# Performance work log

Measured on AMD Instinct MI355X. Metric: run time of the kernel, lower is better.

The kernel has to match this reference:

```python
import jax, jax.numpy as jnp
import numpy as np

NUM_USERS = 50000
NUM_ITEMS = 20000
NUM_NODES = NUM_USERS + NUM_ITEMS
FEAT_DIM = 768
HID = 128
NUM_LAYERS = 3
N_EDGES = 2_000_000
LN_EPS = 1e-5


def setup_inputs() -> dict:
    key = jax.random.key(0)
    ks = jax.random.split(key, 12)
    edge_index = jax.random.randint(ks[0], (2, N_EDGES), 0, NUM_NODES, dtype=jnp.int64) if jax.config.jax_enable_x64 else jax.random.randint(ks[0], (2, N_EDGES), 0, NUM_NODES, dtype=jnp.int32)
    item_features = jax.random.normal(ks[1], (NUM_ITEMS, FEAT_DIM), dtype=jnp.float32)
    embedding = jax.random.normal(ks[2], (NUM_NODES, HID), dtype=jnp.float32) * 0.1
    W1 = jax.random.normal(ks[3], (FEAT_DIM, 512), dtype=jnp.float32) * 0.02
    b1 = jnp.zeros((512,), jnp.float32)
    g1 = jnp.ones((512,), jnp.float32)
    be1 = jnp.zeros((512,), jnp.float32)
    W2 = jax.random.normal(ks[4], (512, HID), dtype=jnp.float32) * 0.02
    b2 = jnp.zeros((HID,), jnp.float32)
    g2 = jnp.ones((HID,), jnp.float32)
    be2 = jnp.zeros((HID,), jnp.float32)
    W3 = jax.random.normal(ks[5], (HID, HID), dtype=jnp.float32) * 0.02
    b3 = jnp.zeros((HID,), jnp.float32)
    meta_weight = jnp.asarray(0.01, jnp.float32)
    return {"edge_index": edge_index, "item_features": item_features, "embedding": embedding,
            "W1": W1, "b1": b1, "g1": g1, "be1": be1,
            "W2": W2, "b2": b2, "g2": g2, "be2": be2,
            "W3": W3, "b3": b3, "meta_weight": meta_weight}


def _layer_norm(x, g, b):
    mu = jnp.mean(x, axis=-1, keepdims=True)
    var = jnp.mean(jnp.square(x - mu), axis=-1, keepdims=True)
    return (x - mu) * jax.lax.rsqrt(var + LN_EPS) * g + b


def reference(edge_index, item_features, embedding, W1, b1, g1, be1, W2, b2, g2, be2, W3, b3, meta_weight):
    # item metadata MLP (eval mode: dropout is identity)
    h = jax.nn.relu(_layer_norm(item_features @ W1 + b1, g1, be1))
    h = jax.nn.relu(_layer_norm(h @ W2 + b2, g2, be2))
    h = h @ W3 + b3
    # F.normalize(p=2, dim=-1)
    item_meta = h / jnp.maximum(jnp.linalg.norm(h, axis=-1, keepdims=True), 1e-12)

    # fuse metadata into item id embeddings
    e0 = jnp.concatenate([embedding[:NUM_USERS],
                          embedding[NUM_USERS:] + meta_weight * item_meta], axis=0)

    src, dst = edge_index[0], edge_index[1]
    # symmetric GCN normalization: deg from destination counts
    deg = jax.ops.segment_sum(jnp.ones(src.shape[0], e0.dtype), dst, num_segments=NUM_NODES)
    dinv = jnp.where(deg > 0, jax.lax.rsqrt(jnp.maximum(deg, 1.0)), 0.0)
    norm = (dinv[src] * dinv[dst])[:, None]  # [E, 1]

    alpha = 1.0 / (NUM_LAYERS + 1)
    out = e0 * alpha
    x = e0
    for _ in range(NUM_LAYERS):
        x = jax.ops.segment_sum(x[src] * norm, dst, num_segments=NUM_NODES)
        out = out + x * alpha
    return out
```

## Files before the change

kernel.cpp:

```cpp
#include <hip/hip_runtime.h>
#include <hip/hip_bf16.h>

#define NUM_USERS 50000
#define NUM_ITEMS 20000
#define NUM_NODES (NUM_USERS + NUM_ITEMS)
#define FEAT_DIM 768
#define HID 128
#define H1DIM 512
#define LN_EPS 1e-5f
#define ALPHA 0.25f
#define NBKT 137

typedef __attribute__((ext_vector_type(8))) short short8;
typedef __attribute__((ext_vector_type(4))) float floatx4;

static __device__ inline unsigned short f2bf(float f) {
  unsigned int u = __float_as_uint(f);
  u += 0x7fffu + ((u >> 16) & 1u);
  return (unsigned short)(u >> 16);
}
static __device__ inline float bflo(unsigned int u) {
  return __uint_as_float(u << 16);
}
static __device__ inline float bfhi(unsigned int u) {
  return __uint_as_float(u & 0xffff0000u);
}

__global__ __launch_bounds__(256) void cast_bf16(
    const float* __restrict__ in, unsigned short* __restrict__ out) {
  size_t i = (size_t)blockIdx.x * 256 + threadIdx.x;
  float4 u = ((const float4*)in)[i * 2];
  float4 v = ((const float4*)in)[i * 2 + 1];
  union { unsigned short s[8]; uint4 q; } p;
  p.s[0] = f2bf(u.x); p.s[1] = f2bf(u.y); p.s[2] = f2bf(u.z); p.s[3] = f2bf(u.w);
  p.s[4] = f2bf(v.x); p.s[5] = f2bf(v.y); p.s[6] = f2bf(v.z); p.s[7] = f2bf(v.w);
  ((uint4*)out)[i] = p.q;
}

__global__ __launch_bounds__(256) void transpose_cast(
    const float* __restrict__ W, unsigned short* __restrict__ Wt,
    int K, int N) {
  __shared__ float tile[32][33];
  int tx = threadIdx.x, ty = threadIdx.y;
  int bx = blockIdx.x, by = blockIdx.y;
#pragma unroll
  for (int kk = 0; kk < 4; kk++)
    tile[ty + kk * 8][tx] = W[(size_t)(by * 32 + ty + kk * 8) * N + bx * 32 + tx];
  __syncthreads();
#pragma unroll
  for (int kk = 0; kk < 4; kk++)
    Wt[(size_t)(bx * 32 + ty + kk * 8) * K + by * 32 + tx] =
        f2bf(tile[tx][ty + kk * 8]);
}

__global__ __launch_bounds__(256) void gemm_mfma_bias(
    const unsigned short* __restrict__ A, const unsigned short* __restrict__ Bt,
    const float* __restrict__ bias, float* __restrict__ C,
    int M, int N, int K) {
  __shared__ __align__(16) unsigned short As[128 * 32];
  __shared__ __align__(16) unsigned short Bs[128 * 32];
  const int tid = threadIdx.x;
  const int wave = tid >> 6, lane = tid & 63;
  const int quad = lane >> 4, l16 = lane & 15;
  const int wm = wave >> 1, wn = wave & 1;
  const int bm = blockIdx.y * 128, bn = blockIdx.x * 128;

  floatx4 acc[4][4];
#pragma unroll
  for (int i = 0; i < 4; i++)
#pragma unroll
    for (int j = 0; j < 4; j++) acc[i][j] = (floatx4){0.f, 0.f, 0.f, 0.f};

  const int srow = lane >> 2;
  const int scol = (lane & 3) * 8;

  for (int k0 = 0; k0 < K; k0 += 32) {
#pragma unroll
    for (int i = 0; i < 2; i++) {
      int c = wave * 2 + i;
      int arow = bm + c * 16 + srow;
      if (arow >= M) arow = M - 1;
      const unsigned short* ga = A + (size_t)arow * K + k0 + scol;
      __builtin_amdgcn_global_load_lds(
          (const __attribute__((address_space(1))) unsigned int*)(uintptr_t)ga,
          (__attribute__((address_space(3))) unsigned int*)(uintptr_t)(As + c * 512),
          16, 0, 0);
      int brow = bn + c * 16 + srow;
      const unsigned short* gb = Bt + (size_t)brow * K + k0 + scol;
      __builtin_amdgcn_global_load_lds(
          (const __attribute__((address_space(1))) unsigned int*)(uintptr_t)gb,
          (__attribute__((address_space(3))) unsigned int*)(uintptr_t)(Bs + c * 512),
          16, 0, 0);
    }
    __syncthreads();

    short8 af[4], bf[4];
#pragma unroll
    for (int i = 0; i < 4; i++) {
      af[i] = *(const short8*)&As[(wm * 64 + i * 16 + l16) * 32 + quad * 8];
      bf[i] = *(const short8*)&Bs[(wn * 64 + i * 16 + l16) * 32 + quad * 8];
    }
#pragma unroll
    for (int i = 0; i < 4; i++)
#pragma unroll
      for (int j = 0; j < 4; j++)
        acc[i][j] = __builtin_amdgcn_mfma_f32_16x16x32_bf16(af[i], bf[j],
                                                            acc[i][j], 0, 0, 0);
    __syncthreads();
  }

#pragma unroll
  for (int i = 0; i < 4; i++) {
    int row0 = bm + wm * 64 + i * 16 + quad * 4;
#pragma unroll
    for (int j = 0; j < 4; j++) {
      int col = bn + wn * 64 + j * 16 + l16;
      float bv = bias[col];
#pragma unroll
      for (int r = 0; r < 4; r++) {
        int row = row0 + r;
        if (row < M) C[(size_t)row * N + col] = acc[i][j][r] + bv;
      }
    }
  }
}

__global__ __launch_bounds__(256) void ln_relu_w512_bf16(
    const float* __restrict__ X, const float* __restrict__ g,
    const float* __restrict__ be, unsigned short* __restrict__ O) {
  int row = blockIdx.x, t = threadIdx.x;
  const float* x = X + (size_t)row * H1DIM;
  float v0 = x[t], v1 = x[t + 256];
  float s = v0 + v1, q = v0 * v0 + v1 * v1;
#pragma unroll
  for (int off = 32; off > 0; off >>= 1) {
    s += __shfl_down(s, off);
    q += __shfl_down(q, off);
  }
  __shared__ float ss[4], qq[4];
  int lane = t & 63, wid = t >> 6;
  if (lane == 0) { ss[wid] = s; qq[wid] = q; }
  __syncthreads();
  float S = ss[0] + ss[1] + ss[2] + ss[3];
  float Q = qq[0] + qq[1] + qq[2] + qq[3];
  float mu = S * (1.f / 512.f);
  float var = Q * (1.f / 512.f) - mu * mu;
  float rs = rsqrtf(var + LN_EPS);
  float y0 = (v0 - mu) * rs * g[t] + be[t];
  float y1 = (v1 - mu) * rs * g[t + 256] + be[t + 256];
  unsigned short* o = O + (size_t)row * H1DIM;
  o[t] = f2bf(fmaxf(y0, 0.f));
  o[t + 256] = f2bf(fmaxf(y1, 0.f));
}

__global__ __launch_bounds__(256) void ln_relu_w128(
    float* __restrict__ X, const float* __restrict__ g,
    const float* __restrict__ be, int rows) {
  int gwid = (blockIdx.x * blockDim.x + threadIdx.x) >> 6;
  if (gwid >= rows) return;
  int lane = threadIdx.x & 63;
  float* x = X + (size_t)gwid * HID;
  float v0 = x[lane], v1 = x[lane + 64];
  float s = v0 + v1, q = v0 * v0 + v1 * v1;
#pragma unroll
  for (int off = 32; off > 0; off >>= 1) {
    s += __shfl_down(s, off);
    q += __shfl_down(q, off);
  }
  s = __shfl(s, 0);
  q = __shfl(q, 0);
  float mu = s * (1.f / 128.f);
  float var = q * (1.f / 128.f) - mu * mu;
  float rs = rsqrtf(var + LN_EPS);
  float y0 = (v0 - mu) * rs * g[lane] + be[lane];
  float y1 = (v1 - mu) * rs * g[lane + 64] + be[lane + 64];
  x[lane] = fmaxf(y0, 0.f);
  x[lane + 64] = fmaxf(y1, 0.f);
}

__global__ __launch_bounds__(128) void gemm3_norm4(
    const float* __restrict__ H, const float* __restrict__ W3,
    const float* __restrict__ b3, float* __restrict__ meta) {
  int r0 = blockIdx.x * 4, t = threadIdx.x;
  __shared__ float hrow[4][HID];
#pragma unroll
  for (int r = 0; r < 4; r++) hrow[r][t] = H[(size_t)(r0 + r) * HID + t];
  __syncthreads();
  float s0 = 0.f, s1 = 0.f, s2 = 0.f, s3 = 0.f;
#pragma unroll 4
  for (int k = 0; k < HID; k++) {
    float w = W3[k * HID + t];
    s0 = fmaf(hrow[0][k], w, s0);
    s1 = fmaf(hrow[1][k], w, s1);
    s2 = fmaf(hrow[2][k], w, s2);
    s3 = fmaf(hrow[3][k], w, s3);
  }
  float b = b3[t];
  s0 += b; s1 += b; s2 += b; s3 += b;
  float q0 = s0 * s0, q1 = s1 * s1, q2 = s2 * s2, q3 = s3 * s3;
#pragma unroll
  for (int off = 32; off > 0; off >>= 1) {
    q0 += __shfl_down(q0, off);
    q1 += __shfl_down(q1, off);
    q2 += __shfl_down(q2, off);
    q3 += __shfl_down(q3, off);
  }
  __shared__ float qs[4][2];
  if ((t & 63) == 0) {
    int w = t >> 6;
    qs[0][w] = q0; qs[1][w] = q1; qs[2][w] = q2; qs[3][w] = q3;
  }
  __syncthreads();
  float n0 = fmaxf(sqrtf(qs[0][0] + qs[0][1]), 1e-12f);
  float n1 = fmaxf(sqrtf(qs[1][0] + qs[1][1]), 1e-12f);
  float n2 = fmaxf(sqrtf(qs[2][0] + qs[2][1]), 1e-12f);
  float n3 = fmaxf(sqrtf(qs[3][0] + qs[3][1]), 1e-12f);
  meta[(size_t)(r0 + 0) * HID + t] = s0 / n0;
  meta[(size_t)(r0 + 1) * HID + t] = s1 / n1;
  meta[(size_t)(r0 + 2) * HID + t] = s2 / n2;
  meta[(size_t)(r0 + 3) * HID + t] = s3 / n3;
}

__global__ __launch_bounds__(256) void build_e0_cm4(
    const float* __restrict__ emb, const float* __restrict__ meta,
    const float* __restrict__ mw_p, const float* __restrict__ dinv,
    unsigned int* __restrict__ x0c, float* __restrict__ out) {
  size_t i = (size_t)blockIdx.x * 256 + threadIdx.x;
  int node = (int)(i >> 6);
  int u6 = (int)(i & 63);
  int chunk = u6 >> 4, fl = u6 & 15;
  int f0 = chunk * 32 + fl * 2;
  float2 e = *(const float2*)&emb[(size_t)node * HID + f0];
  if (node >= NUM_USERS) {
    float2 m = *(const float2*)&meta[(size_t)(node - NUM_USERS) * HID + f0];
    float w = mw_p[0];
    e.x += w * m.x;
    e.y += w * m.y;
  }
  *(float2*)&out[(size_t)node * HID + f0] = make_float2(ALPHA * e.x, ALPHA * e.y);
  float d = dinv[node];
  unsigned pk = (unsigned)f2bf(d * e.x) | ((unsigned)f2bf(d * e.y) << 16);
  x0c[((size_t)chunk * NUM_NODES + node) * 16 + fl] = pk;
}

__global__ __launch_bounds__(256) void p1_hist(const int* __restrict__ dst,
                                               int* __restrict__ ghist,
                                               int E, int NBL) {
  __shared__ int h[NBKT];
  int t = threadIdx.x;
  if (t < NBKT) h[t] = 0;
  __syncthreads();
  int base = blockIdx.x * 8192;
  for (int i = t; i < 8192; i += 256) {
    int e = base + i;
    if (e < E) atomicAdd(&h[dst[e] >> 9], 1);
  }
  __syncthreads();
  if (t < NBKT) ghist[t * NBL + blockIdx.x] = h[t];
}

__global__ __launch_bounds__(256) void scan_a(const int* __restrict__ in,
                                              int* __restrict__ outp,
                                              int* __restrict__ bsum, int n) {
  int i = blockIdx.x * 256 + threadIdx.x;
  int v = (i < n) ? in[i] : 0;
  int lane = threadIdx.x & 63, wid = threadIdx.x >> 6;
  int s = v;
#pragma unroll
  for (int off = 1; off < 64; off <<= 1) {
    int u = __shfl_up(s, off);
    if (lane >= off) s += u;
  }
  __shared__ int wsum[4];
  if (lane == 63) wsum[wid] = s;
  __syncthreads();
  int add = 0;
  for (int w = 0; w < wid; w++) add += wsum[w];
  int incl = s + add;
  if (i < n) outp[i] = incl - v;
  if (threadIdx.x == 255) bsum[blockIdx.x] = incl;
}

__global__ __launch_bounds__(512) void scan_b(int* __restrict__ bsum, int nb) {
  int t = threadIdx.x;
  int v = (t < nb) ? bsum[t] : 0;
  int lane = t & 63, wid = t >> 6;
  int s = v;
#pragma unroll
  for (int off = 1; off < 64; off <<= 1) {
    int u = __shfl_up(s, off);
    if (lane >= off) s += u;
  }
  __shared__ int ws[8];
  if (lane == 63) ws[wid] = s;
  __syncthreads();
  int add = 0;
  for (int w = 0; w < wid; w++) add += ws[w];
  if (t < nb) bsum[t] = s + add - v;
}

__global__ __launch_bounds__(256) void scan_c(int* __restrict__ outp,
                                              const int* __restrict__ bsum,
                                              int n) {
  int i = blockIdx.x * 256 + threadIdx.x;
  if (i < n) outp[i] += bsum[blockIdx.x];
}

__global__ __launch_bounds__(256) void p1_scatter(
    const int* __restrict__ src, const int* __restrict__ dst,
    const int* __restrict__ gscan, unsigned long long* __restrict__ pairs,
    int E, int NBL) {
  __shared__ int cur[NBKT];
  int t = threadIdx.x;
  if (t < NBKT) cur[t] = gscan[t * NBL + blockIdx.x];
  __syncthreads();
  int base = blockIdx.x * 8192;
  for (int i = t; i < 8192; i += 256) {
    int e = base + i;
    if (e < E) {
      int d = dst[e];
      int pos = atomicAdd(&cur[d >> 9], 1);
      pairs[pos] = ((unsigned long long)(unsigned)d << 32) | (unsigned)src[e];
    }
  }
}

__global__ __launch_bounds__(512) void p2_build(
    const unsigned long long* __restrict__ pairs,
    const int* __restrict__ gscan, int* __restrict__ rowptr,
    int* __restrict__ csr_src, int E, int NBL) {
  __shared__ int hist[512];
  __shared__ int ws8[8];
  int b = blockIdx.x, t = threadIdx.x;
  int base = gscan[b * NBL];
  int end = (b == NBKT - 1) ? E : gscan[(b + 1) * NBL];
  hist[t] = 0;
  __syncthreads();
  for (int i = base + t; i < end; i += 512) {
    unsigned d = (unsigned)(pairs[i] >> 32);
    atomicAdd(&hist[d & 511], 1);
  }
  __syncthreads();
  int v = hist[t];
  int lane = t & 63, wid = t >> 6;
  int s = v;
#pragma unroll
  for (int off = 1; off < 64; off <<= 1) {
    int u = __shfl_up(s, off);
    if (lane >= off) s += u;
  }
  if (lane == 63) ws8[wid] = s;
  __syncthreads();
  int add = 0;
  for (int w = 0; w < wid; w++) add += ws8[w];
  int excl = s + add - v;
  int node = (b << 9) + t;
  if (node < NUM_NODES) rowptr[node] = base + excl;
  if (b == NBKT - 1 && t == 0) rowptr[NUM_NODES] = E;
  __syncthreads();
  hist[t] = base + excl;
  __syncthreads();
  for (int i = base + t; i < end; i += 512) {
    unsigned long long p = pairs[i];
    unsigned d = (unsigned)(p >> 32);
    int pos = atomicAdd(&hist[d & 511], 1);
    csr_src[pos] = (int)(unsigned)p;
  }
}

__global__ __launch_bounds__(256) void calc_dinv2(const int* __restrict__ rowptr,
                                                  float* __restrict__ dinv,
                                                  int n) {
  int i = blockIdx.x * 256 + threadIdx.x;
  if (i < n) {
    int d = rowptr[i + 1] - rowptr[i];
    dinv[i] = d > 0 ? rsqrtf((float)d) : 0.f;
  }
}

#define ACC1(v)                 \
  {                             \
    a0 += bflo((v).x);          \
    a1 += bfhi((v).x);          \
    a2 += bflo((v).y);          \
    a3 += bfhi((v).y);          \
  }

__global__ __launch_bounds__(256) void spmm_chunk4(
    const int* __restrict__ rowptr, const int* __restrict__ csrc,
    const float* __restrict__ dinv, const uint2* __restrict__ xc,
    uint2* __restrict__ yc, float* __restrict__ out, int write_y) {
  int chunk = blockIdx.x & 3;
  int rowblk = blockIdx.x >> 2;
  int tid = threadIdx.x;
  int wave = tid >> 6, lane = tid & 63;
  int slot = lane >> 3, fl = lane & 7;
  int row = rowblk * 32 + wave * 8 + slot;
  bool act = row < NUM_NODES;
  int rr = act ? row : NUM_NODES - 1;
  int beg = rowptr[rr], end = rowptr[rr + 1];
  float wd = dinv[rr];
  const uint2* xq = xc + (size_t)chunk * NUM_NODES * 8 + fl;
  float a0 = 0.f, a1 = 0.f, a2 = 0.f, a3 = 0.f;
  int p = beg;
  int na = (beg + 3) & ~3;
  if (na > end) na = end;
  for (; p < na; p++) {
    int s = csrc[p];
    uint2 v = xq[(size_t)(unsigned)s * 8];
    ACC1(v)
  }
  for (; p + 8 <= end; p += 8) {
    uint4 sA = *(const uint4*)(csrc + p);
    uint4 sB = *(const uint4*)(csrc + p + 4);
    uint2 v0 = xq[(size_t)sA.x * 8];
    uint2 v1 = xq[(size_t)sA.y * 8];
    uint2 v2 = xq[(size_t)sA.z * 8];
    uint2 v3 = xq[(size_t)sA.w * 8];
    uint2 v4 = xq[(size_t)sB.x * 8];
    uint2 v5 = xq[(size_t)sB.y * 8];
    uint2 v6 = xq[(size_t)sB.z * 8];
    uint2 v7 = xq[(size_t)sB.w * 8];
    ACC1(v0) ACC1(v1) ACC1(v2) ACC1(v3)
    ACC1(v4) ACC1(v5) ACC1(v6) ACC1(v7)
  }
  if (p + 4 <= end) {
    uint4 sA = *(const uint4*)(csrc + p);
    uint2 v0 = xq[(size_t)sA.x * 8];
    uint2 v1 = xq[(size_t)sA.y * 8];
    uint2 v2 = xq[(size_t)sA.z * 8];
    uint2 v3 = xq[(size_t)sA.w * 8];
    ACC1(v0) ACC1(v1) ACC1(v2) ACC1(v3)
    p += 4;
  }
  for (; p < end; p++) {
    int s = csrc[p];
    uint2 v = xq[(size_t)(unsigned)s * 8];
    ACC1(v)
  }
  float y0 = wd * a0, y1 = wd * a1, y2 = wd * a2, y3 = wd * a3;
  if (act) {
    if (write_y) {
      unsigned p0 = (unsigned)f2bf(wd * y0) | ((unsigned)f2bf(wd * y1) << 16);
      unsigned p1 = (unsigned)f2bf(wd * y2) | ((unsigned)f2bf(wd * y3) << 16);
      yc[((size_t)chunk * NUM_NODES + row) * 8 + fl] = make_uint2(p0, p1);
    }
    float4* op = (float4*)&out[(size_t)row * HID + chunk * 32 + fl * 4];
    float4 po = *op;
    po.x += ALPHA * y0;
    po.y += ALPHA * y1;
    po.z += ALPHA * y2;
    po.w += ALPHA * y3;
    *op = po;
  }
}

extern "C" void kernel_launch(void* const* d_in, const int* in_sizes, int n_in,
                              void* d_out, int out_size, void* d_ws,
                              size_t ws_size, hipStream_t stream) {
  const int* edge = (const int*)d_in[0];
  const float* item_feat = (const float*)d_in[1];
  const float* emb = (const float*)d_in[2];
  const float* W1 = (const float*)d_in[3];
  const float* b1 = (const float*)d_in[4];
  const float* g1 = (const float*)d_in[5];
  const float* be1 = (const float*)d_in[6];
  const float* W2 = (const float*)d_in[7];
  const float* b2 = (const float*)d_in[8];
  const float* g2 = (const float*)d_in[9];
  const float* be2 = (const float*)d_in[10];
  const float* W3 = (const float*)d_in[11];
  const float* b3 = (const float*)d_in[12];
  const float* mw = (const float*)d_in[13];
  float* out = (float*)d_out;

  const int E = in_sizes[0] / 2;
  const int* src = edge;
  const int* dst = edge + E;
  const int NBL = (E + 8191) / 8192;
  const int nScan = NBKT * NBL;
  const int NBs = (nScan + 255) / 256;

  char* ws = (char*)d_ws;
  float* h1 = (float*)(ws + 0);
  float* h2 = (float*)(ws + 40960000);
  unsigned short* h1b = (unsigned short*)(ws + 51200000);
  uint2* xA = (uint2*)(ws + 51200000);
  unsigned short* Af = (unsigned short*)(ws + 87040000);
  uint2* xB = (uint2*)(ws + 87040000);
  uint2* xC = (uint2*)(ws + 104960000);
  unsigned short* W1t = (unsigned short*)(ws + 122880000);
  unsigned short* W2t = (unsigned short*)(ws + 123666432);
  float* meta = (float*)(ws + 26000000);

  unsigned long long* pairs = (unsigned long long*)(ws + 0);
  int* rowptr = (int*)(ws + 16000000);
  float* dinv = (float*)(ws + 16500000);
  int* ghist = (int*)(ws + 16800000);
  int* gscan = (int*)(ws + 17000000);
  int* bsum = (int*)(ws + 17200000);
  int* csr_src = (int*)(ws + 17500000);

  cast_bf16<<<(NUM_ITEMS * FEAT_DIM / 8) / 256, 256, 0, stream>>>(item_feat, Af);
  transpose_cast<<<dim3(H1DIM / 32, FEAT_DIM / 32), dim3(32, 8), 0, stream>>>(
      W1, W1t, FEAT_DIM, H1DIM);
  transpose_cast<<<dim3(HID / 32, H1DIM / 32), dim3(32, 8), 0, stream>>>(
      W2, W2t, H1DIM, HID);

  gemm_mfma_bias<<<dim3(H1DIM / 128, (NUM_ITEMS + 127) / 128), 256, 0, stream>>>(
      Af, W1t, b1, h1, NUM_ITEMS, H1DIM, FEAT_DIM);
  ln_relu_w512_bf16<<<NUM_ITEMS, 256, 0, stream>>>(h1, g1, be1, h1b);
  gemm_mfma_bias<<<dim3(HID / 128, (NUM_ITEMS + 127) / 128), 256, 0, stream>>>(
      h1b, W2t, b2, h2, NUM_ITEMS, HID, H1DIM);
  ln_relu_w128<<<(NUM_ITEMS * 64) / 256, 256, 0, stream>>>(h2, g2, be2,
                                                           NUM_ITEMS);
  gemm3_norm4<<<NUM_ITEMS / 4, 128, 0, stream>>>(h2, W3, b3, meta);

  p1_hist<<<NBL, 256, 0, stream>>>(dst, ghist, E, NBL);
  scan_a<<<NBs, 256, 0, stream>>>(ghist, gscan, bsum, nScan);
  scan_b<<<1, 512, 0, stream>>>(bsum, NBs);
  scan_c<<<NBs, 256, 0, stream>>>(gscan, bsum, nScan);
  p1_scatter<<<NBL, 256, 0, stream>>>(src, dst, gscan, pairs, E, NBL);
  p2_build<<<NBKT, 512, 0, stream>>>(pairs, gscan, rowptr, csr_src, E, NBL);
  calc_dinv2<<<(NUM_NODES + 255) / 256, 256, 0, stream>>>(rowptr, dinv,
                                                          NUM_NODES);

  build_e0_cm4<<<(NUM_NODES * 64) / 256, 256, 0, stream>>>(
      emb, meta, mw, dinv, (unsigned int*)xA, out);

  const int RG = ((NUM_NODES + 31) / 32) * 4;
  spmm_chunk4<<<RG, 256, 0, stream>>>(rowptr, csr_src, dinv, xA, xB, out, 1);
  spmm_chunk4<<<RG, 256, 0, stream>>>(rowptr, csr_src, dinv, xB, xC, out, 1);
  spmm_chunk4<<<RG, 256, 0, stream>>>(rowptr, csr_src, dinv, xC, nullptr, out, 0);
}
```

Baseline: 571.0 us.

## Sort rows by degree and split SpMM features into eight chunks

Adds a counting sort of nodes by in-degree (histogram, scan, scatter) and builds per-row descriptors so each wave processes rows of similar length, reducing divergence from uneven degrees. The feature layout changes from 4 chunks of 32 features to 8 chunks of 16, which shrinks the per-chunk gather working set so it fits better in cache. The out load is also hoisted ahead of the gather loop. This adds several small preprocessing kernels and scatters output writes by permuted row order.

```diff
diff --git a/kernel.cpp b/kernel.cpp
--- a/kernel.cpp
+++ b/kernel.cpp
@@ -221,15 +221,15 @@
   meta[(size_t)(r0 + 3) * HID + t] = s3 / n3;
 }
 
-__global__ __launch_bounds__(256) void build_e0_cm4(
+__global__ __launch_bounds__(256) void build_e0_cm8(
     const float* __restrict__ emb, const float* __restrict__ meta,
     const float* __restrict__ mw_p, const float* __restrict__ dinv,
     unsigned int* __restrict__ x0c, float* __restrict__ out) {
   size_t i = (size_t)blockIdx.x * 256 + threadIdx.x;
   int node = (int)(i >> 6);
   int u6 = (int)(i & 63);
-  int chunk = u6 >> 4, fl = u6 & 15;
-  int f0 = chunk * 32 + fl * 2;
+  int chunk = u6 >> 3, fl8 = u6 & 7;
+  int f0 = chunk * 16 + fl8 * 2;
   float2 e = *(const float2*)&emb[(size_t)node * HID + f0];
   if (node >= NUM_USERS) {
     float2 m = *(const float2*)&meta[(size_t)(node - NUM_USERS) * HID + f0];
@@ -240,7 +240,7 @@
   *(float2*)&out[(size_t)node * HID + f0] = make_float2(ALPHA * e.x, ALPHA * e.y);
   float d = dinv[node];
   unsigned pk = (unsigned)f2bf(d * e.x) | ((unsigned)f2bf(d * e.y) << 16);
-  x0c[((size_t)chunk * NUM_NODES + node) * 16 + fl] = pk;
+  x0c[((size_t)chunk * NUM_NODES + node) * 8 + fl8] = pk;
 }
 
 __global__ __launch_bounds__(256) void p1_hist(const int* __restrict__ dst,
@@ -378,6 +378,77 @@
   }
 }
 
+__global__ __launch_bounds__(256) void zero_dhist(int* __restrict__ dhist) {
+  dhist[threadIdx.x] = 0;
+}
+
+__global__ __launch_bounds__(256) void deg_hist(const int* __restrict__ rowptr,
+                                                int* __restrict__ dhist, int n) {
+  __shared__ int h[256];
+  int t = threadIdx.x;
+  h[t] = 0;
+  __syncthreads();
+  int i = blockIdx.x * 256 + t;
+  if (i < n) {
+    int deg = rowptr[i + 1] - rowptr[i];
+    if (deg > 255) deg = 255;
+    atomicAdd(&h[deg], 1);
+  }
+  __syncthreads();
+  if (h[t]) atomicAdd(&dhist[t], h[t]);
+}
+
+__global__ __launch_bounds__(256) void deg_scan(const int* __restrict__ dhist,
+                                                int* __restrict__ dcur) {
+  int t = threadIdx.x;
+  int v = dhist[t];
+  int lane = t & 63, wid = t >> 6;
+  int s = v;
+#pragma unroll
+  for (int off = 1; off < 64; off <<= 1) {
+    int u = __shfl_up(s, off);
+    if (lane >= off) s += u;
+  }
+  __shared__ int ws[4];
+  if (lane == 63) ws[wid] = s;
+  __syncthreads();
+  int add = 0;
+  for (int w = 0; w < wid; w++) add += ws[w];
+  dcur[t] = s + add - v;
+}
+
+__global__ __launch_bounds__(256) void deg_scatter(const int* __restrict__ rowptr,
+                                                   int* __restrict__ dcur,
+                                                   int* __restrict__ perm, int n) {
+  __shared__ int lh[256], lb[256];
+  int t = threadIdx.x;
+  lh[t] = 0;
+  __syncthreads();
+  int i = blockIdx.x * 256 + t;
+  int bin = 0, myo = 0;
+  bool a = i < n;
+  if (a) {
+    int deg = rowptr[i + 1] - rowptr[i];
+    bin = deg > 255 ? 255 : deg;
+    myo = atomicAdd(&lh[bin], 1);
+  }
+  __syncthreads();
+  lb[t] = lh[t] ? atomicAdd(&dcur[t], lh[t]) : 0;
+  __syncthreads();
+  if (a) perm[lb[bin] + myo] = i;
+}
+
+__global__ __launch_bounds__(256) void build_rowdesc(
+    const int* __restrict__ perm, const int* __restrict__ rowptr,
+    const float* __restrict__ dinv, uint4* __restrict__ rowdesc, int n) {
+  int i = blockIdx.x * 256 + threadIdx.x;
+  if (i < n) {
+    int r = perm[i];
+    rowdesc[i] = make_uint4((unsigned)rowptr[r], (unsigned)rowptr[r + 1],
+                            __float_as_uint(dinv[r]), (unsigned)r);
+  }
+}
+
 #define ACC1(v)                 \
   {                             \
     a0 += bflo((v).x);          \
@@ -386,56 +457,62 @@
     a3 += bfhi((v).y);          \
   }
 
-__global__ __launch_bounds__(256) void spmm_chunk4(
-    const int* __restrict__ rowptr, const int* __restrict__ csrc,
-    const float* __restrict__ dinv, const uint2* __restrict__ xc,
-    uint2* __restrict__ yc, float* __restrict__ out, int write_y) {
-  int chunk = blockIdx.x & 3;
-  int rowblk = blockIdx.x >> 2;
+__global__ __launch_bounds__(256) void spmm_chunk8(
+    const uint4* __restrict__ rowdesc, const int* __restrict__ csrc,
+    const uint2* __restrict__ xc, uint2* __restrict__ yc,
+    float* __restrict__ out, int write_y) {
+  int chunk = blockIdx.x & 7;
+  int rowblk = blockIdx.x >> 3;
   int tid = threadIdx.x;
   int wave = tid >> 6, lane = tid & 63;
-  int slot = lane >> 3, fl = lane & 7;
-  int row = rowblk * 32 + wave * 8 + slot;
-  bool act = row < NUM_NODES;
-  int rr = act ? row : NUM_NODES - 1;
-  int beg = rowptr[rr], end = rowptr[rr + 1];
-  float wd = dinv[rr];
-  const uint2* xq = xc + (size_t)chunk * NUM_NODES * 8 + fl;
+  int slot = lane >> 2, fl = lane & 3;
+  int rowIdx = rowblk * 64 + wave * 16 + slot;
+  bool act = rowIdx < NUM_NODES;
+  int ri = act ? rowIdx : NUM_NODES - 1;
+  uint4 d = rowdesc[ri];
+  int beg = (int)d.x, end = (int)d.y;
+  if (!act) { beg = 0; end = 0; }
+  float wd = __uint_as_float(d.z);
+  int row = (int)d.w;
+  const uint2* xq = xc + (size_t)chunk * NUM_NODES * 4 + fl;
+  float4* op = (float4*)&out[(size_t)row * HID + chunk * 16 + fl * 4];
+  float4 po = make_float4(0.f, 0.f, 0.f, 0.f);
+  if (act) po = *op;
   float a0 = 0.f, a1 = 0.f, a2 = 0.f, a3 = 0.f;
   int p = beg;
   int na = (beg + 3) & ~3;
   if (na > end) na = end;
   for (; p < na; p++) {
     int s = csrc[p];
-    uint2 v = xq[(size_t)(unsigned)s * 8];
+    uint2 v = xq[(size_t)(unsigned)s * 4];
     ACC1(v)
   }
   for (; p + 8 <= end; p += 8) {
     uint4 sA = *(const uint4*)(csrc + p);
     uint4 sB = *(const uint4*)(csrc + p + 4);
-    uint2 v0 = xq[(size_t)sA.x * 8];
-    uint2 v1 = xq[(size_t)sA.y * 8];
-    uint2 v2 = xq[(size_t)sA.z * 8];
-    uint2 v3 = xq[(size_t)sA.w * 8];
-    uint2 v4 = xq[(size_t)sB.x * 8];
-    uint2 v5 = xq[(size_t)sB.y * 8];
-    uint2 v6 = xq[(size_t)sB.z * 8];
-    uint2 v7 = xq[(size_t)sB.w * 8];
+    uint2 v0 = xq[(size_t)sA.x * 4];
+    uint2 v1 = xq[(size_t)sA.y * 4];
+    uint2 v2 = xq[(size_t)sA.z * 4];
+    uint2 v3 = xq[(size_t)sA.w * 4];
+    uint2 v4 = xq[(size_t)sB.x * 4];
+    uint2 v5 = xq[(size_t)sB.y * 4];
+    uint2 v6 = xq[(size_t)sB.z * 4];
+    uint2 v7 = xq[(size_t)sB.w * 4];
     ACC1(v0) ACC1(v1) ACC1(v2) ACC1(v3)
     ACC1(v4) ACC1(v5) ACC1(v6) ACC1(v7)
   }
   if (p + 4 <= end) {
     uint4 sA = *(const uint4*)(csrc + p);
-    uint2 v0 = xq[(size_t)sA.x * 8];
-    uint2 v1 = xq[(size_t)sA.y * 8];
-    uint2 v2 = xq[(size_t)sA.z * 8];
-    uint2 v3 = xq[(size_t)sA.w * 8];
+    uint2 v0 = xq[(size_t)sA.x * 4];
+    uint2 v1 = xq[(size_t)sA.y * 4];
+    uint2 v2 = xq[(size_t)sA.z * 4];
+    uint2 v3 = xq[(size_t)sA.w * 4];
     ACC1(v0) ACC1(v1) ACC1(v2) ACC1(v3)
     p += 4;
   }
   for (; p < end; p++) {
     int s = csrc[p];
-    uint2 v = xq[(size_t)(unsigned)s * 8];
+    uint2 v = xq[(size_t)(unsigned)s * 4];
     ACC1(v)
   }
   float y0 = wd * a0, y1 = wd * a1, y2 = wd * a2, y3 = wd * a3;
@@ -443,10 +520,8 @@
     if (write_y) {
       unsigned p0 = (unsigned)f2bf(wd * y0) | ((unsigned)f2bf(wd * y1) << 16);
       unsigned p1 = (unsigned)f2bf(wd * y2) | ((unsigned)f2bf(wd * y3) << 16);
-      yc[((size_t)chunk * NUM_NODES + row) * 8 + fl] = make_uint2(p0, p1);
+      yc[((size_t)chunk * NUM_NODES + row) * 4 + fl] = make_uint2(p0, p1);
     }
-    float4* op = (float4*)&out[(size_t)row * HID + chunk * 32 + fl * 4];
-    float4 po = *op;
     po.x += ALPHA * y0;
     po.y += ALPHA * y1;
     po.z += ALPHA * y2;
@@ -500,6 +575,10 @@
   int* gscan = (int*)(ws + 17000000);
   int* bsum = (int*)(ws + 17200000);
   int* csr_src = (int*)(ws + 17500000);
+  int* perm = (int*)(ws + 36500000);
+  uint4* rowdesc = (uint4*)(ws + 36800000);
+  int* dhist = (int*)(ws + 38000000);
+  int* dcur = (int*)(ws + 38002048);
 
   cast_bf16<<<(NUM_ITEMS * FEAT_DIM / 8) / 256, 256, 0, stream>>>(item_feat, Af);
   transpose_cast<<<dim3(H1DIM / 32, FEAT_DIM / 32), dim3(32, 8), 0, stream>>>(
@@ -525,11 +604,19 @@
   calc_dinv2<<<(NUM_NODES + 255) / 256, 256, 0, stream>>>(rowptr, dinv,
                                                           NUM_NODES);
 
-  build_e0_cm4<<<(NUM_NODES * 64) / 256, 256, 0, stream>>>(
+  const int NB70 = (NUM_NODES + 255) / 256;
+  zero_dhist<<<1, 256, 0, stream>>>(dhist);
+  deg_hist<<<NB70, 256, 0, stream>>>(rowptr, dhist, NUM_NODES);
+  deg_scan<<<1, 256, 0, stream>>>(dhist, dcur);
+  deg_scatter<<<NB70, 256, 0, stream>>>(rowptr, dcur, perm, NUM_NODES);
+  build_rowdesc<<<NB70, 256, 0, stream>>>(perm, rowptr, dinv, rowdesc,
+                                          NUM_NODES);
+
+  build_e0_cm8<<<(NUM_NODES * 64) / 256, 256, 0, stream>>>(
       emb, meta, mw, dinv, (unsigned int*)xA, out);
 
-  const int RG = ((NUM_NODES + 31) / 32) * 4;
-  spmm_chunk4<<<RG, 256, 0, stream>>>(rowptr, csr_src, dinv, xA, xB, out, 1);
-  spmm_chunk4<<<RG, 256, 0, stream>>>(rowptr, csr_src, dinv, xB, xC, out, 1);
-  spmm_chunk4<<<RG, 256, 0, stream>>>(rowptr, csr_src, dinv, xC, nullptr, out, 0);
-}
+  const int RG8 = ((NUM_NODES + 63) / 64) * 8;
+  spmm_chunk8<<<RG8, 256, 0, stream>>>(rowdesc, csr_src, xA, xB, out, 1);
+  spmm_chunk8<<<RG8, 256, 0, stream>>>(rowdesc, csr_src, xB, xC, out, 1);
+  spmm_chunk8<<<RG8, 256, 0, stream>>>(rowdesc, csr_src, xC, nullptr, out, 0);
+}
```

Result: slower. 707.2 us (+23.9%).

## Split CSR rows into two source-range halves to improve gather locality

Applied to the files above, without the earlier changes.

The CSR build now sorts each row's neighbors into two groups, sources below and above a split index, and stores two offsets per row. The SpMM walks the low-source half first, then the high-source half. The goal is for concurrently running waves to gather from a smaller, more cache-resident slice of the feature array. In exchange, each row pays for a second loop pass with its own alignment prologue and tail handling, the rowptr array doubles in size, and the build kernel uses twice the shared histogram.

```diff
diff --git a/kernel.cpp b/kernel.cpp
--- a/kernel.cpp
+++ b/kernel.cpp
@@ -10,6 +10,7 @@
 #define LN_EPS 1e-5f
 #define ALPHA 0.25f
 #define NBKT 137
+#define SPLIT 35000
 
 typedef __attribute__((ext_vector_type(8))) short short8;
 typedef __attribute__((ext_vector_type(4))) float floatx4;
@@ -325,25 +326,29 @@
   }
 }
 
-__global__ __launch_bounds__(512) void p2_build(
+__global__ __launch_bounds__(512) void p2_build2(
     const unsigned long long* __restrict__ pairs,
-    const int* __restrict__ gscan, int* __restrict__ rowptr,
+    const int* __restrict__ gscan, int* __restrict__ rowptr2,
     int* __restrict__ csr_src, int E, int NBL) {
-  __shared__ int hist[512];
+  __shared__ int hist[1024];
   __shared__ int ws8[8];
   int b = blockIdx.x, t = threadIdx.x;
   int base = gscan[b * NBL];
   int end = (b == NBKT - 1) ? E : gscan[(b + 1) * NBL];
   hist[t] = 0;
+  hist[t + 512] = 0;
   __syncthreads();
   for (int i = base + t; i < end; i += 512) {
-    unsigned d = (unsigned)(pairs[i] >> 32);
-    atomicAdd(&hist[d & 511], 1);
-  }
-  __syncthreads();
-  int v = hist[t];
+    unsigned long long p = pairs[i];
+    unsigned d = (unsigned)(p >> 32);
+    unsigned s = (unsigned)p;
+    atomicAdd(&hist[((d & 511) << 1) | (s >= SPLIT)], 1);
+  }
+  __syncthreads();
+  int v0 = hist[2 * t], v1 = hist[2 * t + 1];
+  int pv = v0 + v1;
   int lane = t & 63, wid = t >> 6;
-  int s = v;
+  int s = pv;
 #pragma unroll
   for (int off = 1; off < 64; off <<= 1) {
     int u = __shfl_up(s, off);
@@ -353,27 +358,33 @@
   __syncthreads();
   int add = 0;
   for (int w = 0; w < wid; w++) add += ws8[w];
-  int excl = s + add - v;
+  int excl = s + add - pv;
+  int p0 = base + excl;
+  int p1 = p0 + v0;
   int node = (b << 9) + t;
-  if (node < NUM_NODES) rowptr[node] = base + excl;
-  if (b == NBKT - 1 && t == 0) rowptr[NUM_NODES] = E;
-  __syncthreads();
-  hist[t] = base + excl;
+  if (node < NUM_NODES) {
+    rowptr2[2 * node] = p0;
+    rowptr2[2 * node + 1] = p1;
+  }
+  if (b == NBKT - 1 && t == 0) rowptr2[2 * NUM_NODES] = E;
+  __syncthreads();
+  hist[2 * t] = p0;
+  hist[2 * t + 1] = p1;
   __syncthreads();
   for (int i = base + t; i < end; i += 512) {
     unsigned long long p = pairs[i];
     unsigned d = (unsigned)(p >> 32);
-    int pos = atomicAdd(&hist[d & 511], 1);
-    csr_src[pos] = (int)(unsigned)p;
-  }
-}
-
-__global__ __launch_bounds__(256) void calc_dinv2(const int* __restrict__ rowptr,
-                                                  float* __restrict__ dinv,
-                                                  int n) {
+    unsigned sv = (unsigned)p;
+    int pos = atomicAdd(&hist[((d & 511) << 1) | (sv >= SPLIT)], 1);
+    csr_src[pos] = (int)sv;
+  }
+}
+
+__global__ __launch_bounds__(256) void calc_dinv2s(
+    const int* __restrict__ rowptr2, float* __restrict__ dinv, int n) {
   int i = blockIdx.x * 256 + threadIdx.x;
   if (i < n) {
-    int d = rowptr[i + 1] - rowptr[i];
+    int d = rowptr2[2 * i + 2] - rowptr2[2 * i];
     dinv[i] = d > 0 ? rsqrtf((float)d) : 0.f;
   }
 }
@@ -386,8 +397,8 @@
     a3 += bfhi((v).y);          \
   }
 
-__global__ __launch_bounds__(256) void spmm_chunk4(
-    const int* __restrict__ rowptr, const int* __restrict__ csrc,
+__global__ __launch_bounds__(256) void spmm_chunk4h(
+    const int* __restrict__ rowptr2, const int* __restrict__ csrc,
     const float* __restrict__ dinv, const uint2* __restrict__ xc,
     uint2* __restrict__ yc, float* __restrict__ out, int write_y) {
   int chunk = blockIdx.x & 3;
@@ -398,45 +409,49 @@
   int row = rowblk * 32 + wave * 8 + slot;
   bool act = row < NUM_NODES;
   int rr = act ? row : NUM_NODES - 1;
-  int beg = rowptr[rr], end = rowptr[rr + 1];
+  int beg = rowptr2[2 * rr], mid = rowptr2[2 * rr + 1], e2 = rowptr2[2 * rr + 2];
   float wd = dinv[rr];
   const uint2* xq = xc + (size_t)chunk * NUM_NODES * 8 + fl;
   float a0 = 0.f, a1 = 0.f, a2 = 0.f, a3 = 0.f;
-  int p = beg;
-  int na = (beg + 3) & ~3;
-  if (na > end) na = end;
-  for (; p < na; p++) {
-    int s = csrc[p];
-    uint2 v = xq[(size_t)(unsigned)s * 8];
-    ACC1(v)
-  }
-  for (; p + 8 <= end; p += 8) {
-    uint4 sA = *(const uint4*)(csrc + p);
-    uint4 sB = *(const uint4*)(csrc + p + 4);
-    uint2 v0 = xq[(size_t)sA.x * 8];
-    uint2 v1 = xq[(size_t)sA.y * 8];
-    uint2 v2 = xq[(size_t)sA.z * 8];
-    uint2 v3 = xq[(size_t)sA.w * 8];
-    uint2 v4 = xq[(size_t)sB.x * 8];
-    uint2 v5 = xq[(size_t)sB.y * 8];
-    uint2 v6 = xq[(size_t)sB.z * 8];
-    uint2 v7 = xq[(size_t)sB.w * 8];
-    ACC1(v0) ACC1(v1) ACC1(v2) ACC1(v3)
-    ACC1(v4) ACC1(v5) ACC1(v6) ACC1(v7)
-  }
-  if (p + 4 <= end) {
-    uint4 sA = *(const uint4*)(csrc + p);
-    uint2 v0 = xq[(size_t)sA.x * 8];
-    uint2 v1 = xq[(size_t)sA.y * 8];
-    uint2 v2 = xq[(size_t)sA.z * 8];
-    uint2 v3 = xq[(size_t)sA.w * 8];
-    ACC1(v0) ACC1(v1) ACC1(v2) ACC1(v3)
-    p += 4;
-  }
-  for (; p < end; p++) {
-    int s = csrc[p];
-    uint2 v = xq[(size_t)(unsigned)s * 8];
-    ACC1(v)
+#pragma unroll 1
+  for (int h = 0; h < 2; h++) {
+    int p = h ? mid : beg;
+    int e = h ? e2 : mid;
+    int na = (p + 3) & ~3;
+    if (na > e) na = e;
+    for (; p < na; p++) {
+      int s = csrc[p];
+      uint2 v = xq[(size_t)(unsigned)s * 8];
+      ACC1(v)
+    }
+    for (; p + 8 <= e; p += 8) {
+      uint4 sA = *(const uint4*)(csrc + p);
+      uint4 sB = *(const uint4*)(csrc + p + 4);
+      uint2 v0 = xq[(size_t)sA.x * 8];
+      uint2 v1 = xq[(size_t)sA.y * 8];
+      uint2 v2 = xq[(size_t)sA.z * 8];
+      uint2 v3 = xq[(size_t)sA.w * 8];
+      uint2 v4 = xq[(size_t)sB.x * 8];
+      uint2 v5 = xq[(size_t)sB.y * 8];
+      uint2 v6 = xq[(size_t)sB.z * 8];
+      uint2 v7 = xq[(size_t)sB.w * 8];
+      ACC1(v0) ACC1(v1) ACC1(v2) ACC1(v3)
+      ACC1(v4) ACC1(v5) ACC1(v6) ACC1(v7)
+    }
+    if (p + 4 <= e) {
+      uint4 sA = *(const uint4*)(csrc + p);
+      uint2 v0 = xq[(size_t)sA.x * 8];
+      uint2 v1 = xq[(size_t)sA.y * 8];
+      uint2 v2 = xq[(size_t)sA.z * 8];
+      uint2 v3 = xq[(size_t)sA.w * 8];
+      ACC1(v0) ACC1(v1) ACC1(v2) ACC1(v3)
+      p += 4;
+    }
+    for (; p < e; p++) {
+      int s = csrc[p];
+      uint2 v = xq[(size_t)(unsigned)s * 8];
+      ACC1(v)
+    }
   }
   float y0 = wd * a0, y1 = wd * a1, y2 = wd * a2, y3 = wd * a3;
   if (act) {
@@ -494,11 +509,11 @@
   float* meta = (float*)(ws + 26000000);
 
   unsigned long long* pairs = (unsigned long long*)(ws + 0);
-  int* rowptr = (int*)(ws + 16000000);
-  float* dinv = (float*)(ws + 16500000);
-  int* ghist = (int*)(ws + 16800000);
-  int* gscan = (int*)(ws + 17000000);
-  int* bsum = (int*)(ws + 17200000);
+  int* rowptr2 = (int*)(ws + 16000000);
+  float* dinv = (float*)(ws + 16600000);
+  int* ghist = (int*)(ws + 16900000);
+  int* gscan = (int*)(ws + 17100000);
+  int* bsum = (int*)(ws + 17300000);
   int* csr_src = (int*)(ws + 17500000);
 
   cast_bf16<<<(NUM_ITEMS * FEAT_DIM / 8) / 256, 256, 0, stream>>>(item_feat, Af);
@@ -521,15 +536,15 @@
   scan_b<<<1, 512, 0, stream>>>(bsum, NBs);
   scan_c<<<NBs, 256, 0, stream>>>(gscan, bsum, nScan);
   p1_scatter<<<NBL, 256, 0, stream>>>(src, dst, gscan, pairs, E, NBL);
-  p2_build<<<NBKT, 512, 0, stream>>>(pairs, gscan, rowptr, csr_src, E, NBL);
-  calc_dinv2<<<(NUM_NODES + 255) / 256, 256, 0, stream>>>(rowptr, dinv,
-                                                          NUM_NODES);
+  p2_build2<<<NBKT, 512, 0, stream>>>(pairs, gscan, rowptr2, csr_src, E, NBL);
+  calc_dinv2s<<<(NUM_NODES + 255) / 256, 256, 0, stream>>>(rowptr2, dinv,
+                                                           NUM_NODES);
 
   build_e0_cm4<<<(NUM_NODES * 64) / 256, 256, 0, stream>>>(
       emb, meta, mw, dinv, (unsigned int*)xA, out);
 
   const int RG = ((NUM_NODES + 31) / 32) * 4;
-  spmm_chunk4<<<RG, 256, 0, stream>>>(rowptr, csr_src, dinv, xA, xB, out, 1);
-  spmm_chunk4<<<RG, 256, 0, stream>>>(rowptr, csr_src, dinv, xB, xC, out, 1);
-  spmm_chunk4<<<RG, 256, 0, stream>>>(rowptr, csr_src, dinv, xC, nullptr, out, 0);
-}
+  spmm_chunk4h<<<RG, 256, 0, stream>>>(rowptr2, csr_src, dinv, xA, xB, out, 1);
+  spmm_chunk4h<<<RG, 256, 0, stream>>>(rowptr2, csr_src, dinv, xB, xC, out, 1);
+  spmm_chunk4h<<<RG, 256, 0, stream>>>(rowptr2, csr_src, dinv, xC, nullptr, out, 0);
+}
```

New measurement: 610.6 us. 1.07x slower.
